# Kernel tuning notes

Measured on AMD Instinct MI355X. Metric: run time of the kernel, lower is better.

The kernel has to match this reference:

```python
import math
import jax, jax.numpy as jnp
import numpy as np

B, T = 2, 2048
D_MODEL, D_HEAD = 2048, 128
N_Q, N_KV = 16, 4
QPG = N_Q // N_KV  # queries per kv group
ROPE_BASE = 10000.0
YARN_SCALE = 4.0
ORIG_MAX_LEN = 4096
BETA_FAST, BETA_SLOW = 32.0, 1.0
RMS_EPS = 1.1920929e-07  # torch.finfo(float32).eps (nn.RMSNorm default)


def _yarn_inv_freq():
    inv = 1.0 / ROPE_BASE ** (np.arange(0, D_HEAD, 2, dtype=np.float32) / D_HEAD)
    wavelengths = 2.0 * math.pi / inv
    low_wavelen = ORIG_MAX_LEN / BETA_SLOW
    high_wavelen = ORIG_MAX_LEN / BETA_FAST
    gamma = np.clip((low_wavelen - wavelengths) / (low_wavelen - high_wavelen), 0.0, 1.0)
    return (gamma * inv + (1.0 - gamma) * inv / YARN_SCALE).astype(np.float32)

INV_FREQ = jnp.asarray(_yarn_inv_freq())  # (D_HEAD//2,) constant buffer
MSCALE = 0.1 * math.log(YARN_SCALE) + 1.0
ATTN_SCALE = 1.0 / (MSCALE * math.sqrt(D_HEAD))


def _rms_norm(x, w):
    # normalize over last dim (d_head), learnable per-dim weight
    return x * jax.lax.rsqrt(jnp.mean(x * x, axis=-1, keepdims=True) + RMS_EPS) * w


def _apply_rope(x):
    # x: (..., T, d_head)
    t = jnp.arange(x.shape[-2], dtype=jnp.float32)
    freqs = jnp.outer(t, INV_FREQ)                 # (T, d/2)
    emb = jnp.concatenate([freqs, freqs], axis=-1)  # (T, d)
    cos, sin = jnp.cos(emb), jnp.sin(emb)
    half = x.shape[-1] // 2
    x_rot = jnp.concatenate([-x[..., half:], x[..., :half]], axis=-1)
    return x * cos + x_rot * sin


def setup_inputs() -> dict:
    key = jax.random.key(0)
    ks = jax.random.split(key, 5)
    x = jax.random.normal(ks[0], (B, T, D_MODEL), dtype=jnp.float32)
    w_scale = 0.02
    Wq = jax.random.normal(ks[1], (D_MODEL, N_Q * D_HEAD), dtype=jnp.float32) * w_scale
    Wkv = jax.random.normal(ks[2], (D_MODEL, 2 * N_KV * D_HEAD), dtype=jnp.float32) * w_scale
    Wo = jax.random.normal(ks[3], (N_Q * D_HEAD, D_MODEL), dtype=jnp.float32) * w_scale
    q_norm_w = jnp.ones((D_HEAD,), dtype=jnp.float32)
    k_norm_w = jnp.ones((D_HEAD,), dtype=jnp.float32)
    return {"x": x, "Wq": Wq, "Wkv": Wkv, "Wo": Wo,
            "q_norm_w": q_norm_w, "k_norm_w": k_norm_w}


def reference(x, Wq, Wkv, Wo, q_norm_w, k_norm_w):
    b, t, _ = x.shape
    # projections
    q = (x @ Wq).reshape(b, t, QPG, N_KV, D_HEAD).transpose(0, 2, 3, 1, 4)  # (b,qpg,g,t,d)
    kv = x @ Wkv
    k, v = jnp.split(kv, 2, axis=-1)
    k = k.reshape(b, t, N_KV, D_HEAD).transpose(0, 2, 1, 3)  # (b,g,t,d)
    v = v.reshape(b, t, N_KV, D_HEAD).transpose(0, 2, 1, 3)  # (b,g,t,d)
    # RMSNorm + YaRN RoPE on q,k (math done in float32 as in source)
    q = _apply_rope(_rms_norm(q, q_norm_w))
    k = _apply_rope(_rms_norm(k, k_norm_w))
    # GQA replication: head index h = qpg*N_KV + g (matches source rearrange/reshape)
    q = q.reshape(b, N_Q, t, D_HEAD)
    k = jnp.broadcast_to(k[:, None], (b, QPG, N_KV, t, D_HEAD)).reshape(b, N_Q, t, D_HEAD)
    v = jnp.broadcast_to(v[:, None], (b, QPG, N_KV, t, D_HEAD)).reshape(b, N_Q, t, D_HEAD)
    # causal SDPA with custom scale
    scores = jnp.einsum('bhtd,bhsd->bhts', q, k) * ATTN_SCALE
    causal = jnp.tril(jnp.ones((t, t), dtype=bool))
    scores = jnp.where(causal, scores, jnp.finfo(scores.dtype).min)
    probs = jax.nn.softmax(scores, axis=-1)
    attn = jnp.einsum('bhts,bhsd->bhtd', probs, v)
    out = attn.transpose(0, 2, 1, 3).reshape(b, t, N_Q * D_HEAD)
    return out @ Wo
```

## Files before the change

### kernel.cpp

```cpp
#include <hip/hip_runtime.h>
#include <cmath>

typedef float f32x4 __attribute__((ext_vector_type(4)));
typedef __bf16 bf16x8 __attribute__((ext_vector_type(8)));

#define DEV static __device__ __forceinline__

DEV unsigned short f2bf(float f) {
  unsigned int u = __builtin_bit_cast(unsigned int, f);
  u += 0x7FFFu + ((u >> 16) & 1u);
  return (unsigned short)(u >> 16);
}
DEV float bf2f(unsigned short h) {
  unsigned int u = ((unsigned int)h) << 16;
  return __builtin_bit_cast(float, u);
}
DEV f32x4 mfma16(bf16x8 a, bf16x8 b, f32x4 c) {
  return __builtin_amdgcn_mfma_f32_16x16x32_bf16(a, b, c, 0, 0, 0);
}
DEV void dma16(const void* g, void* l) {
  __builtin_amdgcn_global_load_lds(
      (const __attribute__((address_space(1))) void*)(uintptr_t)g,
      (__attribute__((address_space(3))) void*)(unsigned int)(uintptr_t)l,
      16, 0, 0);
}

constexpr int T_SEQ = 2048;

__global__ __launch_bounds__(256) void build_rope(float2* __restrict__ rope) {
  int gid = blockIdx.x * 256 + threadIdx.x;
  if (gid >= T_SEQ * 64) return;
  int t = gid >> 6, i = gid & 63;
  double inv = pow(10000.0, -((double)(2 * i)) / 128.0);
  double wl = 6.283185307179586 / inv;
  double gm = (4096.0 - wl) / (4096.0 - 128.0);
  gm = gm < 0.0 ? 0.0 : (gm > 1.0 ? 1.0 : gm);
  float f = (float)(gm * inv + (1.0 - gm) * inv * 0.25);
  float th = (float)t * f;
  float s, c;
  sincosf(th, &s, &c);
  rope[gid] = make_float2(c, s);
}

__global__ __launch_bounds__(256) void cvt_f32_bf16(const float4* __restrict__ in,
                                                    ushort* __restrict__ out, int n4) {
  int i = blockIdx.x * 256 + threadIdx.x;
  if (i >= n4) return;
  float4 v = in[i];
  unsigned int lo = (unsigned int)f2bf(v.x) | ((unsigned int)f2bf(v.y) << 16);
  unsigned int hi = (unsigned int)f2bf(v.z) | ((unsigned int)f2bf(v.w) << 16);
  int row = i >> 9;
  int e = (i * 4) & 2047;
  size_t o = ((size_t)row << 11) + (size_t)(e ^ ((row & 7) << 3));
  *(uint2*)(out + o) = make_uint2(lo, hi);
}

__global__ __launch_bounds__(256) void tconv(const float* __restrict__ in,
                                             ushort* __restrict__ out, int R, int C) {
  __shared__ ushort tile[64][65];
  int c0 = blockIdx.x * 64, r0 = blockIdx.y * 64;
  int j = threadIdx.x & 63, i0 = threadIdx.x >> 6;
#pragma unroll
  for (int ii = 0; ii < 16; ++ii) {
    int i = i0 + ii * 4;
    tile[i][j] = f2bf(in[(size_t)(r0 + i) * C + c0 + j]);
  }
  __syncthreads();
#pragma unroll
  for (int ii = 0; ii < 16; ++ii) {
    int jr = i0 + ii * 4;
    out[(size_t)(c0 + jr) * R + ((r0 + j) ^ ((jr & 7) << 3))] = tile[j][jr];
  }
}

template <int OUT_BF16>
__global__ __launch_bounds__(256) void gemm_bt(const ushort* __restrict__ A,
                                               const ushort* __restrict__ Bt,
                                               void* __restrict__ Cv,
                                               int M, int N, int K) {
  __shared__ ushort lA[128 * 64];
  __shared__ ushort lB[128 * 64];
  const int tid = threadIdx.x;
  const int lane = tid & 63;
  const int w = tid >> 6;
  const int m0 = blockIdx.y * 128;
  const int n0 = blockIdx.x * 128;
  const int wm = (w >> 1) << 6;
  const int wn = (w & 1) << 6;

  f32x4 acc[4][4] = {};

  const size_t K2 = (size_t)K * 2;
  const char* Ab = (const char*)A + (size_t)m0 * K2;
  const char* Bb = (const char*)Bt + (size_t)n0 * K2;
  const int drow = w * 32 + (lane >> 3);
  const int dcb = (lane & 7) * 16;

  for (int k0 = 0; k0 < K; k0 += 64) {
#pragma unroll
    for (int ii = 0; ii < 4; ++ii) {
      const int off = w * 4096 + ii * 1024;
      const size_t gofs = (size_t)(drow + ii * 8) * K2 + (size_t)k0 * 2 + dcb;
      dma16(Ab + gofs, (char*)lA + off);
      dma16(Bb + gofs, (char*)lB + off);
    }
    __syncthreads();
#pragma unroll
    for (int kc = 0; kc < 2; ++kc) {
      bf16x8 a[4], bb[4];
#pragma unroll
      for (int mt = 0; mt < 4; ++mt) {
        int row = wm + mt * 16 + (lane & 15);
        int byo = kc * 64 + ((lane >> 4) << 4);
        a[mt] = *(const bf16x8*)((const char*)lA + row * 128 + (byo ^ ((row & 7) << 4)));
      }
#pragma unroll
      for (int nt = 0; nt < 4; ++nt) {
        int row = wn + nt * 16 + (lane & 15);
        int byo = kc * 64 + ((lane >> 4) << 4);
        bb[nt] = *(const bf16x8*)((const char*)lB + row * 128 + (byo ^ ((row & 7) << 4)));
      }
#pragma unroll
      for (int mt = 0; mt < 4; ++mt)
#pragma unroll
        for (int nt = 0; nt < 4; ++nt)
          acc[mt][nt] = mfma16(a[mt], bb[nt], acc[mt][nt]);
    }
    __syncthreads();
  }

  const int rr = (lane >> 4) << 2;
  const int cc = lane & 15;
  if (OUT_BF16) {
    ushort* C = (ushort*)Cv;
#pragma unroll
    for (int mt = 0; mt < 4; ++mt)
#pragma unroll
      for (int nt = 0; nt < 4; ++nt)
#pragma unroll
        for (int j = 0; j < 4; ++j) {
          int r = m0 + wm + mt * 16 + rr + j;
          int c = n0 + wn + nt * 16 + cc;
          C[(size_t)r * N + c] = f2bf(acc[mt][nt][j]);
        }
  } else {
    float* C = (float*)Cv;
#pragma unroll
    for (int mt = 0; mt < 4; ++mt)
#pragma unroll
      for (int nt = 0; nt < 4; ++nt)
#pragma unroll
        for (int j = 0; j < 4; ++j) {
          int r = m0 + wm + mt * 16 + rr + j;
          int c = n0 + wn + nt * 16 + cc;
          C[(size_t)r * N + c] = acc[mt][nt][j];
        }
  }
}

__global__ __launch_bounds__(256) void norm_rope(const ushort* __restrict__ qkv,
                                                 const float* __restrict__ qw,
                                                 const float* __restrict__ kw,
                                                 const float2* __restrict__ rope,
                                                 ushort* __restrict__ qout,
                                                 ushort* __restrict__ kout,
                                                 float attn_scale) {
  const int w = threadIdx.x >> 6, lane = threadIdx.x & 63;
  const int vi = blockIdx.x * 4 + w;
  const ushort* src;
  const float* wt;
  ushort* dst;
  float extra;
  int t, bb;
  if (vi < 65536) {
    int row = vi >> 4, H = vi & 15;
    bb = row >> 11;
    t = row & 2047;
    src = qkv + (size_t)row * 3072 + H * 128 + lane * 2;
    wt = qw;
    extra = attn_scale;
    dst = qout + ((size_t)(bb * 16 + H) * T_SEQ + t) * 128 + lane * 2;
  } else {
    int vi2 = vi - 65536;
    int row = vi2 >> 2, gg = vi2 & 3;
    bb = row >> 11;
    t = row & 2047;
    src = qkv + (size_t)row * 3072 + 2048 + gg * 128 + lane * 2;
    wt = kw;
    extra = 1.f;
    dst = kout + ((size_t)(bb * 4 + gg) * T_SEQ + t) * 128 +
          ((lane * 2) ^ ((t & 7) << 3));
  }
  float x0 = bf2f(src[0]), x1 = bf2f(src[1]);
  float ss = x0 * x0 + x1 * x1;
#pragma unroll
  for (int d = 1; d < 64; d <<= 1) ss += __shfl_xor(ss, d, 64);
  float sc = rsqrtf(ss * (1.f / 128.f) + 1.1920929e-7f);
  float w0 = wt[lane * 2], w1 = wt[lane * 2 + 1];
  float xn0 = x0 * sc * w0, xn1 = x1 * sc * w1;
  float p0 = __shfl_xor(xn0, 32, 64), p1 = __shfl_xor(xn1, 32, 64);
  float r0 = lane < 32 ? -p0 : p0;
  float r1 = lane < 32 ? -p1 : p1;
  int i0 = (lane * 2) & 63;
  float2 cs0 = rope[t * 64 + i0];
  float2 cs1 = rope[t * 64 + i0 + 1];
  float o0 = (xn0 * cs0.x + r0 * cs0.y) * extra;
  float o1 = (xn1 * cs1.x + r1 * cs1.y) * extra;
  unsigned int pk = (unsigned int)f2bf(o0) | ((unsigned int)f2bf(o1) << 16);
  *(unsigned int*)dst = pk;
}

__global__ __launch_bounds__(256) void tv_kernel(const ushort* __restrict__ qkv,
                                                 ushort* __restrict__ vt) {
  __shared__ ushort tile[64][65];
  int t0 = blockIdx.x * 64;
  int y = blockIdx.y;
  int dh = y & 1, bg = y >> 1;
  int bb = bg >> 2, g = bg & 3;
  int j = threadIdx.x & 63, i0 = threadIdx.x >> 6;
#pragma unroll
  for (int ii = 0; ii < 16; ++ii) {
    int i = i0 + ii * 4;
    tile[i][j] = qkv[(size_t)(bb * T_SEQ + t0 + i) * 3072 + 2560 + g * 128 + dh * 64 + j];
  }
  __syncthreads();
#pragma unroll
  for (int ii = 0; ii < 16; ++ii) {
    int jr = i0 + ii * 4;
    vt[((size_t)bg * 128 + dh * 64 + jr) * T_SEQ + ((t0 + j) ^ ((jr & 7) << 3))] = tile[j][jr];
  }
}

__global__ __launch_bounds__(256, 4) void attn_fwd(const ushort* __restrict__ qh,
                                                   const ushort* __restrict__ kh,
                                                   const ushort* __restrict__ vt,
                                                   ushort* __restrict__ o) {
  const int f = blockIdx.x;
  const int r = f >> 8, kk = (f >> 5) & 7, bh = f & 31;
  const int qt = (r == 0) ? (31 - kk) : (r == 1) ? (16 + kk) : (r == 2) ? (15 - kk) : kk;
  const int b = bh >> 4, H = bh & 15;
  const int g = H & 3;
  const int tid = threadIdx.x, lane = tid & 63, w = tid >> 6;
  const int wrow0 = qt * 64 + w * 16;

  __shared__ ushort lK[64 * 128];
  __shared__ ushort lV[128 * 64];
  __shared__ ushort lP[4 * 16 * 64];

  bf16x8 qf[4];
  {
    const ushort* qb = qh + ((size_t)(b * 16 + H) * T_SEQ + wrow0 + (lane & 15)) * 128 +
                       ((lane >> 4) << 3);
#pragma unroll
    for (int kc = 0; kc < 4; ++kc) qf[kc] = *(const bf16x8*)(qb + kc * 32);
  }

  f32x4 oacc[8] = {};
  float mrow = -INFINITY, lrow = 0.f;

  const char* kpl = (const char*)(kh + (size_t)(b * 4 + g) * T_SEQ * 128);
  const char* vpl = (const char*)(vt + (size_t)(b * 4 + g) * 128 * T_SEQ);

  auto stage = [&](int j) {
#pragma unroll
    for (int ii = 0; ii < 4; ++ii) {
      const int off = w * 4096 + ii * 1024;
      dma16(kpl + (size_t)j * 16384 + off + lane * 16, (char*)lK + off);
      const int vrow = w * 32 + ii * 8 + (lane >> 3);
      dma16(vpl + (size_t)vrow * (T_SEQ * 2) + j * 128 + (lane & 7) * 16, (char*)lV + off);
    }
  };

  stage(0);

  const int qrow = wrow0 + (lane & 15);
  const int rsel = ((lane >> 4) << 2);

  for (int j = 0; j <= qt; ++j) {
    asm volatile("s_waitcnt vmcnt(0)" ::: "memory");
    __builtin_amdgcn_s_barrier();
    __builtin_amdgcn_sched_barrier(0);

    f32x4 s[4];
#pragma unroll
    for (int nt = 0; nt < 4; ++nt) {
      bf16x8 kf[4];
      int krow = nt * 16 + (lane & 15);
#pragma unroll
      for (int kc = 0; kc < 4; ++kc) {
        int byo = kc * 64 + ((lane >> 4) << 4);
        kf[kc] = *(const bf16x8*)((const char*)lK + krow * 256 + (byo ^ ((krow & 7) << 4)));
      }
      f32x4 a = {0.f, 0.f, 0.f, 0.f};
#pragma unroll
      for (int kc = 0; kc < 4; ++kc) a = mfma16(kf[kc], qf[kc], a);
      s[nt] = a;
    }

    if (j == qt) {
#pragma unroll
      for (int nt = 0; nt < 4; ++nt)
#pragma unroll
        for (int jj = 0; jj < 4; ++jj) {
          int col = j * 64 + nt * 16 + ((lane >> 4) << 2) + jj;
          if (col > qrow) s[nt][jj] = -3.0e38f;
        }
    }

    float pm0 = fmaxf(fmaxf(s[0][0], s[0][1]), fmaxf(s[0][2], s[0][3]));
    float pm1 = fmaxf(fmaxf(s[1][0], s[1][1]), fmaxf(s[1][2], s[1][3]));
    float pm2 = fmaxf(fmaxf(s[2][0], s[2][1]), fmaxf(s[2][2], s[2][3]));
    float pm3 = fmaxf(fmaxf(s[3][0], s[3][1]), fmaxf(s[3][2], s[3][3]));
    float pm = fmaxf(fmaxf(pm0, pm1), fmaxf(pm2, pm3));
    pm = fmaxf(pm, __shfl_xor(pm, 16, 64));
    pm = fmaxf(pm, __shfl_xor(pm, 32, 64));

    float mn = mrow;
    if (!__all(pm <= mrow + 8.f)) {
      mn = fmaxf(mrow, pm);
      float rsc = __expf(mrow - mn);
      mrow = mn;
      lrow *= rsc;
      float rr0 = __shfl(rsc, rsel + 0, 64);
      float rr1 = __shfl(rsc, rsel + 1, 64);
      float rr2 = __shfl(rsc, rsel + 2, 64);
      float rr3 = __shfl(rsc, rsel + 3, 64);
#pragma unroll
      for (int dt = 0; dt < 8; ++dt) {
        oacc[dt][0] *= rr0; oacc[dt][1] *= rr1;
        oacc[dt][2] *= rr2; oacc[dt][3] *= rr3;
      }
    }

    float ps = 0.f;
#pragma unroll
    for (int nt = 0; nt < 4; ++nt) {
      float p0 = __expf(s[nt][0] - mn);
      float p1 = __expf(s[nt][1] - mn);
      float p2 = __expf(s[nt][2] - mn);
      float p3 = __expf(s[nt][3] - mn);
      ps += (p0 + p1) + (p2 + p3);
      unsigned int w0 = (unsigned int)f2bf(p0) | ((unsigned int)f2bf(p1) << 16);
      unsigned int w1 = (unsigned int)f2bf(p2) | ((unsigned int)f2bf(p3) << 16);
      int prow = lane & 15;
      int pcb = (nt * 32 + ((lane >> 4) << 3)) ^ ((prow & 7) << 4);
      *(uint2*)((char*)lP + w * 2048 + prow * 128 + pcb) = make_uint2(w0, w1);
    }
    ps += __shfl_xor(ps, 16, 64);
    ps += __shfl_xor(ps, 32, 64);
    lrow += ps;

#pragma unroll
    for (int kc2 = 0; kc2 < 2; ++kc2) {
      int prow = lane & 15;
      int pbo = kc2 * 64 + ((lane >> 4) << 4);
      bf16x8 pa = *(const bf16x8*)((char*)lP + w * 2048 + prow * 128 +
                                   (pbo ^ ((prow & 7) << 4)));
#pragma unroll
      for (int dt = 0; dt < 8; ++dt) {
        int vrow = dt * 16 + (lane & 15);
        int vbo = kc2 * 64 + ((lane >> 4) << 4);
        bf16x8 vf = *(const bf16x8*)((const char*)lV + vrow * 128 + (vbo ^ ((vrow & 7) << 4)));
        oacc[dt] = mfma16(pa, vf, oacc[dt]);
      }
    }

    __builtin_amdgcn_sched_barrier(0);
    __builtin_amdgcn_s_barrier();
    if (j < qt) stage(j + 1);
  }

  float linv = 1.f / lrow;
  float iv0 = __shfl(linv, rsel + 0, 64);
  float iv1 = __shfl(linv, rsel + 1, 64);
  float iv2 = __shfl(linv, rsel + 2, 64);
  float iv3 = __shfl(linv, rsel + 3, 64);
#pragma unroll
  for (int dt = 0; dt < 8; ++dt) {
    float v0 = oacc[dt][0] * iv0, v1 = oacc[dt][1] * iv1;
    float v2 = oacc[dt][2] * iv2, v3 = oacc[dt][3] * iv3;
    int col = H * 128 + dt * 16 + (lane & 15);
    int row = wrow0 + rsel;
    o[(size_t)(b * T_SEQ + row + 0) * 2048 + (col ^ (((row + 0) & 7) << 3))] = f2bf(v0);
    o[(size_t)(b * T_SEQ + row + 1) * 2048 + (col ^ (((row + 1) & 7) << 3))] = f2bf(v1);
    o[(size_t)(b * T_SEQ + row + 2) * 2048 + (col ^ (((row + 2) & 7) << 3))] = f2bf(v2);
    o[(size_t)(b * T_SEQ + row + 3) * 2048 + (col ^ (((row + 3) & 7) << 3))] = f2bf(v3);
  }
}

extern "C" void kernel_launch(void* const* d_in, const int* in_sizes, int n_in,
                              void* d_out, int out_size, void* d_ws, size_t ws_size,
                              hipStream_t stream) {
  (void)in_sizes; (void)n_in; (void)out_size; (void)ws_size;
  const float* x = (const float*)d_in[0];
  const float* Wq = (const float*)d_in[1];
  const float* Wkv = (const float*)d_in[2];
  const float* Wo = (const float*)d_in[3];
  const float* qnw = (const float*)d_in[4];
  const float* knw = (const float*)d_in[5];
  float* out = (float*)d_out;
  char* ws = (char*)d_ws;

  ushort* xb = (ushort*)(ws);
  ushort* wqkv = (ushort*)(ws + 16777216);
  ushort* wot = (ushort*)(ws + 29360128);
  ushort* qkvraw = (ushort*)(ws + 37748736);
  ushort* kh = (ushort*)(ws + 62914560);
  ushort* vtp = (ushort*)(ws + 67108864);
  float2* rope = (float2*)(ws + 71303168);
  ushort* qh = xb;
  ushort* attnb = qkvraw;

  float attn_scale = 1.0f / ((0.1f * logf(4.0f) + 1.0f) * sqrtf(128.0f));

  build_rope<<<512, 256, 0, stream>>>(rope);
  cvt_f32_bf16<<<8192, 256, 0, stream>>>((const float4*)x, xb, 2097152);
  tconv<<<dim3(32, 32), 256, 0, stream>>>(Wq, wqkv, 2048, 2048);
  tconv<<<dim3(16, 32), 256, 0, stream>>>(Wkv, wqkv + (size_t)2048 * 2048, 2048, 1024);
  tconv<<<dim3(32, 32), 256, 0, stream>>>(Wo, wot, 2048, 2048);
  gemm_bt<1><<<dim3(24, 32), 256, 0, stream>>>(xb, wqkv, qkvraw, 4096, 3072, 2048);
  norm_rope<<<20480, 256, 0, stream>>>(qkvraw, qnw, knw, rope, qh, kh, attn_scale);
  tv_kernel<<<dim3(32, 16), 256, 0, stream>>>(qkvraw, vtp);
  attn_fwd<<<1024, 256, 0, stream>>>(qh, kh, vtp, attnb);
  gemm_bt<0><<<dim3(16, 32), 256, 0, stream>>>(attnb, wot, out, 4096, 2048, 2048);
}
```

Before: 227.5 us.

## Double-buffer K/V staging with 512-thread attention blocks and exp2 softmax

The attention kernel now runs 8 waves per block over a 128-row query tile, shares each K/V tile across twice as many query rows, and double-buffers the K/V LDS stages so the next tile's DMA is issued before computing on the current one. The log2(e) factor is folded into the Q scaling so softmax uses exp2f, and the rescale threshold is adjusted to match. LDS use roughly doubles and the grid halves to 512 blocks, which may reduce occupancy and load balance across CUs. The causal mask now also applies per wave on the diagonal tiles.

Result: no change. 229.4 us (+0.9%).

```diff
diff --git a/kernel.cpp b/kernel.cpp
--- a/kernel.cpp
+++ b/kernel.cpp
@@ -164,7 +164,7 @@
                                                  const float2* __restrict__ rope,
                                                  ushort* __restrict__ qout,
                                                  ushort* __restrict__ kout,
-                                                 float attn_scale) {
+                                                 float q_scale) {
   const int w = threadIdx.x >> 6, lane = threadIdx.x & 63;
   const int vi = blockIdx.x * 4 + w;
   const ushort* src;
@@ -178,7 +178,7 @@
     t = row & 2047;
     src = qkv + (size_t)row * 3072 + H * 128 + lane * 2;
     wt = qw;
-    extra = attn_scale;
+    extra = q_scale;
     dst = qout + ((size_t)(bb * 16 + H) * T_SEQ + t) * 128 + lane * 2;
   } else {
     int vi2 = vi - 65536;
@@ -231,21 +231,22 @@
   }
 }
 
-__global__ __launch_bounds__(256, 4) void attn_fwd(const ushort* __restrict__ qh,
+__global__ __launch_bounds__(512, 4) void attn_fwd(const ushort* __restrict__ qh,
                                                    const ushort* __restrict__ kh,
                                                    const ushort* __restrict__ vt,
                                                    ushort* __restrict__ o) {
   const int f = blockIdx.x;
-  const int r = f >> 8, kk = (f >> 5) & 7, bh = f & 31;
-  const int qt = (r == 0) ? (31 - kk) : (r == 1) ? (16 + kk) : (r == 2) ? (15 - kk) : kk;
+  const int half = f >> 8, c = f & 255;
+  const int kk = c >> 5, bh = c & 31;
+  const int qt = half ? kk : (15 - kk);
   const int b = bh >> 4, H = bh & 15;
   const int g = H & 3;
   const int tid = threadIdx.x, lane = tid & 63, w = tid >> 6;
-  const int wrow0 = qt * 64 + w * 16;
-
-  __shared__ ushort lK[64 * 128];
-  __shared__ ushort lV[128 * 64];
-  __shared__ ushort lP[4 * 16 * 64];
+  const int wrow0 = qt * 128 + w * 16;
+
+  __shared__ ushort lK[2][64 * 128];
+  __shared__ ushort lV[2][128 * 64];
+  __shared__ ushort lP[8 * 16 * 64];
 
   bf16x8 qf[4];
   {
@@ -261,23 +262,31 @@
   const char* kpl = (const char*)(kh + (size_t)(b * 4 + g) * T_SEQ * 128);
   const char* vpl = (const char*)(vt + (size_t)(b * 4 + g) * 128 * T_SEQ);
 
-  auto stage = [&](int j) {
-#pragma unroll
-    for (int ii = 0; ii < 4; ++ii) {
-      const int off = w * 4096 + ii * 1024;
-      dma16(kpl + (size_t)j * 16384 + off + lane * 16, (char*)lK + off);
-      const int vrow = w * 32 + ii * 8 + (lane >> 3);
-      dma16(vpl + (size_t)vrow * (T_SEQ * 2) + j * 128 + (lane & 7) * 16, (char*)lV + off);
+  auto stage = [&](int j, int bi) {
+#pragma unroll
+    for (int ii = 0; ii < 2; ++ii) {
+      const int off = w * 2048 + ii * 1024;
+      dma16(kpl + (size_t)j * 16384 + off + lane * 16, (char*)lK[bi] + off);
+      const int vrow = w * 16 + ii * 8 + (lane >> 3);
+      dma16(vpl + (size_t)vrow * (T_SEQ * 2) + j * 128 + (lane & 7) * 16,
+            (char*)lV[bi] + off);
     }
   };
 
-  stage(0);
+  stage(0, 0);
 
   const int qrow = wrow0 + (lane & 15);
   const int rsel = ((lane >> 4) << 2);
 
-  for (int j = 0; j <= qt; ++j) {
-    asm volatile("s_waitcnt vmcnt(0)" ::: "memory");
+  const int jmax = 2 * qt + 1;
+  for (int j = 0; j <= jmax; ++j) {
+    const int cur = j & 1;
+    if (j < jmax) {
+      stage(j + 1, cur ^ 1);
+      asm volatile("s_waitcnt vmcnt(4)" ::: "memory");
+    } else {
+      asm volatile("s_waitcnt vmcnt(0)" ::: "memory");
+    }
     __builtin_amdgcn_s_barrier();
     __builtin_amdgcn_sched_barrier(0);
 
@@ -289,7 +298,7 @@
 #pragma unroll
       for (int kc = 0; kc < 4; ++kc) {
         int byo = kc * 64 + ((lane >> 4) << 4);
-        kf[kc] = *(const bf16x8*)((const char*)lK + krow * 256 + (byo ^ ((krow & 7) << 4)));
+        kf[kc] = *(const bf16x8*)((const char*)lK[cur] + krow * 256 + (byo ^ ((krow & 7) << 4)));
       }
       f32x4 a = {0.f, 0.f, 0.f, 0.f};
 #pragma unroll
@@ -297,7 +306,7 @@
       s[nt] = a;
     }
 
-    if (j == qt) {
+    if (j * 64 + 63 > wrow0) {
 #pragma unroll
       for (int nt = 0; nt < 4; ++nt)
 #pragma unroll
@@ -316,9 +325,9 @@
     pm = fmaxf(pm, __shfl_xor(pm, 32, 64));
 
     float mn = mrow;
-    if (!__all(pm <= mrow + 8.f)) {
+    if (!__all(pm <= mrow + 11.5417f)) {
       mn = fmaxf(mrow, pm);
-      float rsc = __expf(mrow - mn);
+      float rsc = exp2f(mrow - mn);
       mrow = mn;
       lrow *= rsc;
       float rr0 = __shfl(rsc, rsel + 0, 64);
@@ -335,10 +344,10 @@
     float ps = 0.f;
 #pragma unroll
     for (int nt = 0; nt < 4; ++nt) {
-      float p0 = __expf(s[nt][0] - mn);
-      float p1 = __expf(s[nt][1] - mn);
-      float p2 = __expf(s[nt][2] - mn);
-      float p3 = __expf(s[nt][3] - mn);
+      float p0 = exp2f(s[nt][0] - mn);
+      float p1 = exp2f(s[nt][1] - mn);
+      float p2 = exp2f(s[nt][2] - mn);
+      float p3 = exp2f(s[nt][3] - mn);
       ps += (p0 + p1) + (p2 + p3);
       unsigned int w0 = (unsigned int)f2bf(p0) | ((unsigned int)f2bf(p1) << 16);
       unsigned int w1 = (unsigned int)f2bf(p2) | ((unsigned int)f2bf(p3) << 16);
@@ -360,14 +369,13 @@
       for (int dt = 0; dt < 8; ++dt) {
         int vrow = dt * 16 + (lane & 15);
         int vbo = kc2 * 64 + ((lane >> 4) << 4);
-        bf16x8 vf = *(const bf16x8*)((const char*)lV + vrow * 128 + (vbo ^ ((vrow & 7) << 4)));
+        bf16x8 vf = *(const bf16x8*)((const char*)lV[cur] + vrow * 128 + (vbo ^ ((vrow & 7) << 4)));
         oacc[dt] = mfma16(pa, vf, oacc[dt]);
       }
     }
 
     __builtin_amdgcn_sched_barrier(0);
     __builtin_amdgcn_s_barrier();
-    if (j < qt) stage(j + 1);
   }
 
   float linv = 1.f / lrow;
@@ -412,6 +420,7 @@
   ushort* attnb = qkvraw;
 
   float attn_scale = 1.0f / ((0.1f * logf(4.0f) + 1.0f) * sqrtf(128.0f));
+  float q_scale = attn_scale * 1.44269504f;
 
   build_rope<<<512, 256, 0, stream>>>(rope);
   cvt_f32_bf16<<<8192, 256, 0, stream>>>((const float4*)x, xb, 2097152);
@@ -419,8 +428,8 @@
   tconv<<<dim3(16, 32), 256, 0, stream>>>(Wkv, wqkv + (size_t)2048 * 2048, 2048, 1024);
   tconv<<<dim3(32, 32), 256, 0, stream>>>(Wo, wot, 2048, 2048);
   gemm_bt<1><<<dim3(24, 32), 256, 0, stream>>>(xb, wqkv, qkvraw, 4096, 3072, 2048);
-  norm_rope<<<20480, 256, 0, stream>>>(qkvraw, qnw, knw, rope, qh, kh, attn_scale);
+  norm_rope<<<20480, 256, 0, stream>>>(qkvraw, qnw, knw, rope, qh, kh, q_scale);
   tv_kernel<<<dim3(32, 16), 256, 0, stream>>>(qkvraw, vtp);
-  attn_fwd<<<1024, 256, 0, stream>>>(qh, kh, vtp, attnb);
+  attn_fwd<<<512, 512, 0, stream>>>(qh, kh, vtp, attnb);
   gemm_bt<0><<<dim3(16, 32), 256, 0, stream>>>(attnb, wot, out, 4096, 2048, 2048);
 }
```
